# Kernel optimization log

Measured on AMD Instinct MI355X. Metric: run time of the kernel, lower is better.

Reference implementation:

```python
import math
import jax, jax.numpy as jnp
import numpy as np

B, C, H, W = 8, 64, 128, 128
KH = KW = 3
PAD = 1
STRIDE = 1
DIL = 1
GROUPS = 4


def setup_inputs() -> dict:
    key = jax.random.key(0)
    k1, k2, k3, k4, k5 = jax.random.split(key, 5)
    x = jax.random.normal(k1, (B, C, H, W), jnp.float32)
    skip = jax.random.normal(k2, (B, C, H, W), jnp.float32)
    # offset-predicting conv: in_channels -> 2*KH*KW (has bias). Small init so offsets are modest.
    offset_w = jax.random.normal(k3, (2 * KH * KW, C, KH, KW), jnp.float32) * 0.01
    offset_b = jax.random.normal(k4, (2 * KH * KW,), jnp.float32) * 0.01
    # deformable conv weight: grouped, no bias. [Cout, Cin//G, KH, KW]
    fan_in = (C // GROUPS) * KH * KW
    deform_w = jax.random.normal(k5, (C, C // GROUPS, KH, KW), jnp.float32) * (1.0 / math.sqrt(fan_in))
    return {"x": x, "skip": skip, "offset_w": offset_w, "offset_b": offset_b, "deform_w": deform_w}


def _conv2d(x, w, b):
    y = jax.lax.conv_general_dilated(
        x, w, window_strides=(STRIDE, STRIDE), padding=((PAD, PAD), (PAD, PAD)),
        rhs_dilation=(DIL, DIL), dimension_numbers=("NCHW", "OIHW", "NCHW"))
    return y + b[None, :, None, None]


def _deform_conv(skip, offsets, w):
    # torchvision DeformConv2d semantics, offset_groups=1, zero-padded bilinear sampling.
    Bn, Cn, Hn, Wn = skip.shape
    Ho, Wo = offsets.shape[2], offsets.shape[3]
    K = KH * KW
    # offsets: [B, 2*K, Ho, Wo] ordered (k, (dy, dx))
    off = offsets.reshape(Bn, K, 2, Ho, Wo)
    off_y, off_x = off[:, :, 0], off[:, :, 1]  # [B,K,Ho,Wo]
    ky, kx = jnp.meshgrid(jnp.arange(KH), jnp.arange(KW), indexing="ij")
    ky, kx = ky.reshape(K), kx.reshape(K)
    base_y = (jnp.arange(Ho) * STRIDE - PAD)[None, None, :, None] + (ky * DIL)[None, :, None, None]
    base_x = (jnp.arange(Wo) * STRIDE - PAD)[None, None, None, :] + (kx * DIL)[None, :, None, None]
    py = base_y + off_y  # [B,K,Ho,Wo] sampling rows
    px = base_x + off_x  # sampling cols
    y0f = jnp.floor(py)
    x0f = jnp.floor(px)
    wy = py - y0f
    wx = px - x0f
    y0 = y0f.astype(jnp.int32)
    x0 = x0f.astype(jnp.int32)
    skip_flat = skip.reshape(Bn, Cn, Hn * Wn)

    def gather(yi, xi):
        valid = ((yi >= 0) & (yi < Hn) & (xi >= 0) & (xi < Wn)).astype(skip.dtype)  # [B,K,Ho,Wo]
        idx = jnp.clip(yi, 0, Hn - 1) * Wn + jnp.clip(xi, 0, Wn - 1)
        v = jax.vmap(lambda f, i: f[:, i])(skip_flat, idx.reshape(Bn, -1))  # [B,C,K*Ho*Wo]
        return v.reshape(Bn, Cn, K, Ho, Wo) * valid[:, None]

    v00 = gather(y0, x0)
    v01 = gather(y0, x0 + 1)
    v10 = gather(y0 + 1, x0)
    v11 = gather(y0 + 1, x0 + 1)
    wy_b = wy[:, None]  # [B,1,K,Ho,Wo]
    wx_b = wx[:, None]
    sampled = (v00 * (1 - wy_b) * (1 - wx_b) + v01 * (1 - wy_b) * wx_b
               + v10 * wy_b * (1 - wx_b) + v11 * wy_b * wx_b)  # [B,C,K,Ho,Wo]
    # grouped contraction with the kernel weights
    G = GROUPS
    Cg = Cn // G
    Cout = w.shape[0]
    Cog = Cout // G
    sampled_g = sampled.reshape(Bn, G, Cg, K, Ho, Wo)
    w_g = w.reshape(G, Cog, Cg, K)
    out = jnp.einsum("bgckhw,gock->bgohw", sampled_g, w_g)
    return out.reshape(Bn, Cout, Ho, Wo)


def reference(x, skip, offset_w, offset_b, deform_w):
    offsets = _conv2d(x, offset_w, offset_b)
    return _deform_conv(skip, offsets, deform_w)
```

## Files before the change

kernel.cpp:

```cpp
#include <hip/hip_runtime.h>

#define Bn    8
#define Cn    64
#define Hn    128
#define Wn    128
#define KK    9
#define OffC  18
#define NG    4
#define Cg    16
#define HW    (Hn*Wn)

#define OFFS_ELEMS (Bn*OffC*HW)
#define WAO_ELEMS  (KK*4*64*8)
#define WAD_ELEMS  (NG*KK*64*8)

#define ROWS  8
#define TR    15
#define NW    8
#define TSTR  132

typedef __attribute__((ext_vector_type(8)))  short short8v;
typedef __attribute__((ext_vector_type(4)))  unsigned int uint4v;
typedef __attribute__((ext_vector_type(16))) float f32x16;

__device__ __forceinline__ unsigned int rne16(float f) {
    unsigned int u = __float_as_uint(f);
    return (u + 0x7FFFu + ((u >> 16) & 1u)) >> 16;
}
__device__ __forceinline__ unsigned int pack2(float lo, float hi) {
    const unsigned int a = rne16(lo);
    unsigned int b = __float_as_uint(hi);
    b = (b + 0x7FFFu + ((b >> 16) & 1u)) & 0xFFFF0000u;
    return b | a;
}

__global__ __launch_bounds__(256) void prep_w_kernel(
    const float* __restrict__ offw, const float* __restrict__ dw,
    unsigned short* __restrict__ wAo, unsigned short* __restrict__ wAd)
{
    const int tid = blockIdx.x * 256 + threadIdx.x;
    const int nth = gridDim.x * 256;
    for (int i = tid; i < WAO_ELEMS; i += nth) {
        const int e    = i & 7;
        const int lane = (i >> 3) & 63;
        const int q    = (i >> 9) & 3;
        const int t    = i >> 11;
        const int o    = lane & 31;
        const int c    = q * 16 + 8 * (lane >> 5) + e;
        const float v  = (o < OffC) ? offw[(o * Cn + c) * KK + t] : 0.f;
        wAo[i] = (unsigned short)rne16(v);
    }
    for (int i = tid; i < WAD_ELEMS; i += nth) {
        const int e    = i & 7;
        const int lane = (i >> 3) & 63;
        const int t    = (i >> 9) % KK;
        const int g    = i / (512 * KK);
        const int o    = lane & 31;
        const int c    = 8 * (lane >> 5) + e;
        const float v  = (o < Cg) ? dw[((g * Cg + o) * Cg + c) * KK + t] : 0.f;
        wAd[i] = (unsigned short)rne16(v);
    }
}

__global__ __launch_bounds__(256, 4) void offset_conv_kernel(
    const float* __restrict__ x, const unsigned short* __restrict__ wAo,
    const float* __restrict__ bias, float* __restrict__ offs)
{
    const int tid  = threadIdx.x;
    const int wv   = tid >> 6;
    const int lane = tid & 63;
    const int p    = lane & 31;
    const int h    = lane >> 5;
    const int b    = blockIdx.y;
    const int r    = blockIdx.x;
    const int col  = wv * 32 + p;

    const float* xb = x + (size_t)b * Cn * HW;

    f32x16 acc;
#pragma unroll
    for (int i = 0; i < 16; ++i) acc[i] = 0.f;

#pragma unroll 1
    for (int q = 0; q < 4; ++q) {
        unsigned int win[4][3][3];
#pragma unroll
        for (int i = 0; i < 4; ++i) {
            const float* xc0 = xb + (size_t)(q * 16 + 8 * h + 2 * i) * HW;
            const float* xc1 = xc0 + HW;
#pragma unroll
            for (int ky = 0; ky < 3; ++ky) {
                const int  y   = r - 1 + ky;
                const bool yok = ((unsigned)y < (unsigned)Hn);
#pragma unroll
                for (int kx = 0; kx < 3; ++kx) {
                    const int  xx = col - 1 + kx;
                    const bool ok = yok && ((unsigned)xx < (unsigned)Wn);
                    const float f0 = ok ? xc0[y * Wn + xx] : 0.f;
                    const float f1 = ok ? xc1[y * Wn + xx] : 0.f;
                    win[i][ky][kx] = pack2(f0, f1);
                }
            }
        }
#pragma unroll
        for (int t = 0; t < KK; ++t) {
            uint4v bw;
            bw[0] = win[0][t / 3][t % 3];
            bw[1] = win[1][t / 3][t % 3];
            bw[2] = win[2][t / 3][t % 3];
            bw[3] = win[3][t / 3][t % 3];
            const short8v bfrag = __builtin_bit_cast(short8v, bw);
            const short8v afrag = *(const short8v*)(wAo + (size_t)(t * 4 + q) * 512 + lane * 8);
            acc = __builtin_amdgcn_mfma_f32_32x32x16_bf16(afrag, bfrag, acc, 0, 0, 0);
        }
    }

    float* ob = offs + ((size_t)b * OffC * Hn + r) * Wn + col;
#pragma unroll
    for (int reg = 0; reg < 16; ++reg) {
        const int o = (reg & 3) + 8 * (reg >> 2) + 4 * h;
        if (o < OffC) ob[(size_t)o * HW] = acc[reg] + bias[o];
    }
}

__global__ __launch_bounds__(512, 4) void deform_kernel(
    const float* __restrict__ skip, const float* __restrict__ offs,
    const unsigned short* __restrict__ wA, float* __restrict__ out)
{
    __shared__ unsigned int tile[NW * TR * TSTR];

    const int tid = threadIdx.x;
    const int g = blockIdx.y & 3;
    const int b = blockIdx.y >> 2;
    const int r0  = blockIdx.x * ROWS;
    const int ylo = max(0, r0 - 3);
    const int yhi = min(Hn - 1, r0 + ROWS + 3);

    const float* sg = skip + (size_t)(b * Cn + g * Cg) * HW;

    for (int i = tid; i < NW * TR * Wn; i += 512) {
        const int w  = i / (TR * Wn);
        const int re = i % (TR * Wn);
        const int ty = re >> 7;
        const int xx = re & 127;
        const int y  = ylo + ty;
        if (y <= yhi) {
            const float f0 = sg[(2 * w)     * HW + y * Wn + xx];
            const float f1 = sg[(2 * w + 1) * HW + y * Wn + xx];
            tile[(w * TR + ty) * TSTR + xx] = pack2(f0, f1);
        }
    }
    __syncthreads();

    const int wv   = tid >> 6;
    const int lane = tid & 63;
    const int p    = lane & 31;
    const int h    = lane >> 5;
    const int r    = r0 + wv;

    const unsigned short* wAg = wA + (size_t)g * (KK * 512) + lane * 8;
    const float* offb = offs + (size_t)b * OffC * HW + r * Wn;

    for (int j = 0; j < 4; ++j) {
        const int col = j * 32 + p;
        f32x16 acc;
#pragma unroll
        for (int i = 0; i < 16; ++i) acc[i] = 0.f;

        const float* offp = offb + col;

#pragma unroll 2
        for (int t = 0; t < KK; ++t) {
            const int ky = t / 3, kx = t % 3;
            const float offy = offp[(2 * t) * HW];
            const float offx = offp[(2 * t + 1) * HW];
            const float pyf = (float)(r - 1 + ky) + offy;
            const float pxf = (float)(col - 1 + kx) + offx;
            const float y0f = floorf(pyf), x0f = floorf(pxf);
            const float wy = pyf - y0f, wx = pxf - x0f;
            const int y0 = (int)y0f, x0 = (int)x0f, y1 = y0 + 1, x1 = x0 + 1;
            const bool vy0 = ((unsigned)y0 < (unsigned)Hn), vy1 = ((unsigned)y1 < (unsigned)Hn);
            const bool vx0 = ((unsigned)x0 < (unsigned)Wn), vx1 = ((unsigned)x1 < (unsigned)Wn);
            const int y0c = min(max(y0, 0), Hn - 1), y1c = min(max(y1, 0), Hn - 1);
            const int x0c = min(max(x0, 0), Wn - 1), x1c = min(max(x1, 0), Wn - 1);
            const float m0 = (1.f - wy) * (1.f - wx) * ((vy0 && vx0) ? 1.f : 0.f);
            const float m1 = (1.f - wy) * wx         * ((vy0 && vx1) ? 1.f : 0.f);
            const float m2 = wy * (1.f - wx)         * ((vy1 && vx0) ? 1.f : 0.f);
            const float m3 = wy * wx                 * ((vy1 && vx1) ? 1.f : 0.f);
            const bool cond = (y0c >= ylo) && (y1c <= yhi);

            float s[8];
            if (cond) {
                const int tr0 = y0c - ylo, tr1 = y1c - ylo;
#pragma unroll
                for (int wi = 0; wi < 4; ++wi) {
                    const unsigned int* tw = tile + ((4 * h + wi) * TR) * TSTR;
                    const unsigned int u00 = tw[tr0 * TSTR + x0c];
                    const unsigned int u01 = tw[tr0 * TSTR + x1c];
                    const unsigned int u10 = tw[tr1 * TSTR + x0c];
                    const unsigned int u11 = tw[tr1 * TSTR + x1c];
                    s[2 * wi]     = __uint_as_float(u00 << 16) * m0 + __uint_as_float(u01 << 16) * m1
                                  + __uint_as_float(u10 << 16) * m2 + __uint_as_float(u11 << 16) * m3;
                    s[2 * wi + 1] = __uint_as_float(u00 & 0xFFFF0000u) * m0 + __uint_as_float(u01 & 0xFFFF0000u) * m1
                                  + __uint_as_float(u10 & 0xFFFF0000u) * m2 + __uint_as_float(u11 & 0xFFFF0000u) * m3;
                }
            } else {
                const int ia0 = y0c * Wn + x0c, ia1 = y0c * Wn + x1c;
                const int ia2 = y1c * Wn + x0c, ia3 = y1c * Wn + x1c;
#pragma unroll
                for (int i = 0; i < 8; ++i) {
                    const float* sc = sg + (8 * h + i) * HW;
                    s[i] = sc[ia0] * m0 + sc[ia1] * m1 + sc[ia2] * m2 + sc[ia3] * m3;
                }
            }

            short8v bfrag;
#pragma unroll
            for (int i = 0; i < 8; ++i) bfrag[i] = (short)rne16(s[i]);
            const short8v afrag = *(const short8v*)(wAg + t * 512);

            acc = __builtin_amdgcn_mfma_f32_32x32x16_bf16(afrag, bfrag, acc, 0, 0, 0);
        }

        float* ob = out + (size_t)(b * Cn + g * Cg) * HW + r * Wn + col;
#pragma unroll
        for (int reg = 0; reg < 8; ++reg) {
            const int o = (reg & 3) + 8 * (reg >> 2) + 4 * h;
            ob[o * HW] = acc[reg];
        }
    }
}

extern "C" void kernel_launch(void* const* d_in, const int* in_sizes, int n_in,
                              void* d_out, int out_size, void* d_ws, size_t ws_size,
                              hipStream_t stream) {
    const float* x        = (const float*)d_in[0];
    const float* skip     = (const float*)d_in[1];
    const float* offset_w = (const float*)d_in[2];
    const float* offset_b = (const float*)d_in[3];
    const float* deform_w = (const float*)d_in[4];
    float* out  = (float*)d_out;

    float* offs = (float*)d_ws;
    unsigned short* wAo = (unsigned short*)(offs + OFFS_ELEMS);
    unsigned short* wAd = wAo + WAO_ELEMS;

    hipLaunchKernelGGL(prep_w_kernel, dim3(8), dim3(256), 0, stream,
                       offset_w, deform_w, wAo, wAd);
    hipLaunchKernelGGL(offset_conv_kernel, dim3(Hn, Bn), dim3(256), 0, stream,
                       x, wAo, offset_b, offs);
    hipLaunchKernelGGL(deform_kernel, dim3(Hn / ROWS, Bn * NG), dim3(512), 0, stream,
                       skip, offs, wAd, out);
}
```

Measured before the change: 89.02 us.

## Split offset-conv channels across waves, shrink deform tiles, use hardware bf16 packing

The offset conv now splits its input-channel quads across wave pairs, covers half the columns per block (grid z=2), and reduces the two partial sums through shared memory. The deform kernel drops to 4 rows per block with an 8-row halo tile, so each wave handles two column chunks instead of four, and the grid doubles. Bilinear interpolation is done on float2 vectors, and manual bf16 rounding is replaced by the v_cvt_pk_bf16_f32 instruction. Launch bounds rise to 6 blocks per CU. The aim is more parallelism and occupancy and fewer conversion instructions. The smaller halo means more samples fall back to global-memory gathers, and the reduction adds a block-wide barrier.

```diff
diff --git a/kernel.cpp b/kernel.cpp
--- a/kernel.cpp
+++ b/kernel.cpp
@@ -1,4 +1,5 @@
 #include <hip/hip_runtime.h>
+#include <hip/hip_bf16.h>
 
 #define Bn    8
 #define Cn    64
@@ -14,24 +15,24 @@
 #define WAO_ELEMS  (KK*4*64*8)
 #define WAD_ELEMS  (NG*KK*64*8)
 
-#define ROWS  8
-#define TR    15
+#define ROWS  4
+#define TR    8
 #define NW    8
 #define TSTR  132
 
 typedef __attribute__((ext_vector_type(8)))  short short8v;
 typedef __attribute__((ext_vector_type(4)))  unsigned int uint4v;
+typedef __attribute__((ext_vector_type(2)))  float f32x2;
 typedef __attribute__((ext_vector_type(16))) float f32x16;
 
 __device__ __forceinline__ unsigned int rne16(float f) {
     unsigned int u = __float_as_uint(f);
     return (u + 0x7FFFu + ((u >> 16) & 1u)) >> 16;
 }
-__device__ __forceinline__ unsigned int pack2(float lo, float hi) {
-    const unsigned int a = rne16(lo);
-    unsigned int b = __float_as_uint(hi);
-    b = (b + 0x7FFFu + ((b >> 16) & 1u)) & 0xFFFF0000u;
-    return b | a;
+__device__ __forceinline__ unsigned int pk2(float lo, float hi) {
+    unsigned int w;
+    asm("v_cvt_pk_bf16_f32 %0, %1, %2" : "=v"(w) : "v"(lo), "v"(hi));
+    return w;
 }
 
 __global__ __launch_bounds__(256) void prep_w_kernel(
@@ -62,10 +63,11 @@
     }
 }
 
-__global__ __launch_bounds__(256, 4) void offset_conv_kernel(
+__global__ __launch_bounds__(256, 6) void offset_conv_kernel(
     const float* __restrict__ x, const unsigned short* __restrict__ wAo,
     const float* __restrict__ bias, float* __restrict__ offs)
 {
+    __shared__ float red[2][64][17];
     const int tid  = threadIdx.x;
     const int wv   = tid >> 6;
     const int lane = tid & 63;
@@ -73,7 +75,9 @@
     const int h    = lane >> 5;
     const int b    = blockIdx.y;
     const int r    = blockIdx.x;
-    const int col  = wv * 32 + p;
+    const int ck   = wv & 1;
+    const int qh   = wv >> 1;
+    const int col  = blockIdx.z * 64 + ck * 32 + p;
 
     const float* xb = x + (size_t)b * Cn * HW;
 
@@ -82,7 +86,8 @@
     for (int i = 0; i < 16; ++i) acc[i] = 0.f;
 
 #pragma unroll 1
-    for (int q = 0; q < 4; ++q) {
+    for (int qq = 0; qq < 2; ++qq) {
+        const int q = 2 * qh + qq;
         unsigned int win[4][3][3];
 #pragma unroll
         for (int i = 0; i < 4; ++i) {
@@ -98,7 +103,7 @@
                     const bool ok = yok && ((unsigned)xx < (unsigned)Wn);
                     const float f0 = ok ? xc0[y * Wn + xx] : 0.f;
                     const float f1 = ok ? xc1[y * Wn + xx] : 0.f;
-                    win[i][ky][kx] = pack2(f0, f1);
+                    win[i][ky][kx] = pk2(f0, f1);
                 }
             }
         }
@@ -115,15 +120,22 @@
         }
     }
 
-    float* ob = offs + ((size_t)b * OffC * Hn + r) * Wn + col;
-#pragma unroll
-    for (int reg = 0; reg < 16; ++reg) {
-        const int o = (reg & 3) + 8 * (reg >> 2) + 4 * h;
-        if (o < OffC) ob[(size_t)o * HW] = acc[reg] + bias[o];
-    }
-}
-
-__global__ __launch_bounds__(512, 4) void deform_kernel(
+    if (qh == 1) {
+#pragma unroll
+        for (int i = 0; i < 16; ++i) red[ck][lane][i] = acc[i];
+    }
+    __syncthreads();
+    if (qh == 0) {
+        float* ob = offs + ((size_t)b * OffC * Hn + r) * Wn + col;
+#pragma unroll
+        for (int reg = 0; reg < 16; ++reg) {
+            const int o = (reg & 3) + 8 * (reg >> 2) + 4 * h;
+            if (o < OffC) ob[(size_t)o * HW] = acc[reg] + red[ck][lane][reg] + bias[o];
+        }
+    }
+}
+
+__global__ __launch_bounds__(512, 6) void deform_kernel(
     const float* __restrict__ skip, const float* __restrict__ offs,
     const unsigned short* __restrict__ wA, float* __restrict__ out)
 {
@@ -133,21 +145,21 @@
     const int g = blockIdx.y & 3;
     const int b = blockIdx.y >> 2;
     const int r0  = blockIdx.x * ROWS;
-    const int ylo = max(0, r0 - 3);
-    const int yhi = min(Hn - 1, r0 + ROWS + 3);
+    const int ylo = max(0, r0 - 2);
+    const int yhi = min(Hn - 1, r0 + ROWS + 1);
 
     const float* sg = skip + (size_t)(b * Cn + g * Cg) * HW;
 
     for (int i = tid; i < NW * TR * Wn; i += 512) {
-        const int w  = i / (TR * Wn);
-        const int re = i % (TR * Wn);
+        const int w  = i >> 10;
+        const int re = i & 1023;
         const int ty = re >> 7;
         const int xx = re & 127;
         const int y  = ylo + ty;
         if (y <= yhi) {
             const float f0 = sg[(2 * w)     * HW + y * Wn + xx];
             const float f1 = sg[(2 * w + 1) * HW + y * Wn + xx];
-            tile[(w * TR + ty) * TSTR + xx] = pack2(f0, f1);
+            tile[(w * TR + ty) * TSTR + xx] = pk2(f0, f1);
         }
     }
     __syncthreads();
@@ -156,13 +168,14 @@
     const int lane = tid & 63;
     const int p    = lane & 31;
     const int h    = lane >> 5;
-    const int r    = r0 + wv;
+    const int r    = r0 + (wv >> 1);
+    const int jb   = (wv & 1) * 2;
 
     const unsigned short* wAg = wA + (size_t)g * (KK * 512) + lane * 8;
     const float* offb = offs + (size_t)b * OffC * HW + r * Wn;
 
-    for (int j = 0; j < 4; ++j) {
-        const int col = j * 32 + p;
+    for (int jj = 0; jj < 2; ++jj) {
+        const int col = (jb + jj) * 32 + p;
         f32x16 acc;
 #pragma unroll
         for (int i = 0; i < 16; ++i) acc[i] = 0.f;
@@ -189,7 +202,7 @@
             const float m3 = wy * wx                 * ((vy1 && vx1) ? 1.f : 0.f);
             const bool cond = (y0c >= ylo) && (y1c <= yhi);
 
-            float s[8];
+            f32x2 sv[4];
             if (cond) {
                 const int tr0 = y0c - ylo, tr1 = y1c - ylo;
 #pragma unroll
@@ -199,24 +212,29 @@
                     const unsigned int u01 = tw[tr0 * TSTR + x1c];
                     const unsigned int u10 = tw[tr1 * TSTR + x0c];
                     const unsigned int u11 = tw[tr1 * TSTR + x1c];
-                    s[2 * wi]     = __uint_as_float(u00 << 16) * m0 + __uint_as_float(u01 << 16) * m1
-                                  + __uint_as_float(u10 << 16) * m2 + __uint_as_float(u11 << 16) * m3;
-                    s[2 * wi + 1] = __uint_as_float(u00 & 0xFFFF0000u) * m0 + __uint_as_float(u01 & 0xFFFF0000u) * m1
-                                  + __uint_as_float(u10 & 0xFFFF0000u) * m2 + __uint_as_float(u11 & 0xFFFF0000u) * m3;
+                    f32x2 c00, c01, c10, c11;
+                    c00[0] = __uint_as_float(u00 << 16); c00[1] = __uint_as_float(u00 & 0xFFFF0000u);
+                    c01[0] = __uint_as_float(u01 << 16); c01[1] = __uint_as_float(u01 & 0xFFFF0000u);
+                    c10[0] = __uint_as_float(u10 << 16); c10[1] = __uint_as_float(u10 & 0xFFFF0000u);
+                    c11[0] = __uint_as_float(u11 << 16); c11[1] = __uint_as_float(u11 & 0xFFFF0000u);
+                    sv[wi] = c00 * m0 + c01 * m1 + c10 * m2 + c11 * m3;
                 }
             } else {
                 const int ia0 = y0c * Wn + x0c, ia1 = y0c * Wn + x1c;
                 const int ia2 = y1c * Wn + x0c, ia3 = y1c * Wn + x1c;
 #pragma unroll
-                for (int i = 0; i < 8; ++i) {
-                    const float* sc = sg + (8 * h + i) * HW;
-                    s[i] = sc[ia0] * m0 + sc[ia1] * m1 + sc[ia2] * m2 + sc[ia3] * m3;
+                for (int wi = 0; wi < 4; ++wi) {
+                    const float* sc0 = sg + (size_t)(8 * h + 2 * wi) * HW;
+                    const float* sc1 = sc0 + HW;
+                    sv[wi][0] = sc0[ia0] * m0 + sc0[ia1] * m1 + sc0[ia2] * m2 + sc0[ia3] * m3;
+                    sv[wi][1] = sc1[ia0] * m0 + sc1[ia1] * m1 + sc1[ia2] * m2 + sc1[ia3] * m3;
                 }
             }
 
-            short8v bfrag;
-#pragma unroll
-            for (int i = 0; i < 8; ++i) bfrag[i] = (short)rne16(s[i]);
+            uint4v bw;
+#pragma unroll
+            for (int wi = 0; wi < 4; ++wi) bw[wi] = pk2(sv[wi][0], sv[wi][1]);
+            const short8v bfrag = __builtin_bit_cast(short8v, bw);
             const short8v afrag = *(const short8v*)(wAg + t * 512);
 
             acc = __builtin_amdgcn_mfma_f32_32x32x16_bf16(afrag, bfrag, acc, 0, 0, 0);
@@ -247,7 +265,7 @@
 
     hipLaunchKernelGGL(prep_w_kernel, dim3(8), dim3(256), 0, stream,
                        offset_w, deform_w, wAo, wAd);
-    hipLaunchKernelGGL(offset_conv_kernel, dim3(Hn, Bn), dim3(256), 0, stream,
+    hipLaunchKernelGGL(offset_conv_kernel, dim3(Hn, Bn, 2), dim3(256), 0, stream,
                        x, wAo, offset_b, offs);
     hipLaunchKernelGGL(deform_kernel, dim3(Hn / ROWS, Bn * NG), dim3(512), 0, stream,
                        skip, offs, wAd, out);
```

After: 141.5 us. +58.9%, slower.
